# Performance work log

Measured on AMD Instinct MI355X. Metric: run time of the kernel, lower is better.

The kernel has to match this reference:

```python
import jax, jax.numpy as jnp
import numpy as np
from jax import lax

B, T, CD = 128, 4096, 2
HID, K = 64, 5
FIN = CD * 3 + 4  # 10 scorer input channels
PAD = K // 2
LEARNED_W = 0.5


def setup_inputs() -> dict:
    key = jax.random.key(0)
    ks = jax.random.split(key, 10)
    trajectory = jax.random.normal(ks[0], (B, T, CD), jnp.float32)
    intervals = jax.random.uniform(ks[1], (B, T), jnp.float32, 0.01, 1.0)
    lengths = jax.random.randint(ks[2], (B,), T // 2, T + 1)
    attention_mask = (jnp.arange(T)[None, :] < lengths[:, None]).astype(jnp.float32)
    observed_mask = (jax.random.uniform(ks[3], (B, T)) > 0.3).astype(jnp.float32)
    w1 = jax.random.normal(ks[4], (HID, FIN, K), jnp.float32) / np.sqrt(FIN * K)
    b1 = jnp.zeros((HID,), jnp.float32)
    w2 = jax.random.normal(ks[5], (HID, HID, K), jnp.float32) / np.sqrt(HID * K)
    b2 = jnp.zeros((HID,), jnp.float32)
    w3 = jax.random.normal(ks[6], (1, HID, 1), jnp.float32) / np.sqrt(HID)
    b3 = jnp.zeros((1,), jnp.float32)
    return dict(trajectory=trajectory, intervals=intervals, attention_mask=attention_mask,
                observed_mask=observed_mask, w1=w1, b1=b1, w2=w2, b2=b2, w3=w3, b3=b3)


def _conv1d(x, w, pad):  # x: [B,C,T], w: [O,I,K]
    return lax.conv_general_dilated(x, w, (1,), [(pad, pad)],
                                    dimension_numbers=('NCH', 'OIH', 'NCH'))


def _safe_norm(v):  # grad-safe L2 norm over last dim, exact forward
    s2 = jnp.sum(v * v, axis=-1)
    return jnp.where(s2 > 0, jnp.sqrt(jnp.where(s2 > 0, s2, 1.0)), 0.0)


def _robust_normalize(values, mask):
    # vectorized version of per-sample 95th-percentile scaling
    valid = mask > 0.5
    n = jnp.sum(valid, axis=1)  # [B] int
    s = jnp.sort(jnp.where(valid, values, jnp.inf), axis=1)  # valid ascending, inf last
    idx = jnp.maximum(1, jnp.ceil(n.astype(jnp.float32) * 0.95).astype(jnp.int32)) - 1
    idx = jnp.clip(idx, 0, T - 1)
    scale = jnp.abs(jnp.take_along_axis(s, idx[:, None], axis=1))[:, 0]
    maxabs = jnp.max(jnp.where(valid, jnp.abs(values), 0.0), axis=1)
    scale = jnp.where(scale < 1e-6, maxabs, scale)
    out = values / jnp.maximum(scale, 1e-6)[:, None]
    out = jnp.where((n > 0)[:, None], out, 0.0)
    return out * mask


def _smooth(scores, mask):  # avg_pool1d k=K stride 1 pad K//2 (count_include_pad=True)
    kern = jnp.full((1, 1, K), 1.0 / K, scores.dtype)
    sm = _conv1d(scores[:, None, :], kern, PAD)[:, 0]
    return sm * mask


def _forward(trajectory, intervals, attention_mask, observed_mask, w1, b1, w2, b2, w3, b3):
    mask = attention_mask
    vm = mask > 0.5
    pm = (vm[:, 1:] & vm[:, :-1]).astype(trajectory.dtype)  # [B,T-1]

    def mdiff3(x):
        d = (x[:, 1:] - x[:, :-1]) * pm[..., None]
        return jnp.concatenate([jnp.zeros_like(x[:, :1]), d], axis=1)

    def mdiff2(x):
        d = (x[:, 1:] - x[:, :-1]) * pm
        return jnp.concatenate([jnp.zeros_like(x[:, :1]), d], axis=1)

    mt = trajectory * mask[..., None]
    coord_diff = mdiff3(mt)
    delta_t = jnp.maximum(intervals[..., None], 1e-3)
    interval_feat = intervals * mask
    velocity = coord_diff / delta_t * mask[..., None]
    acceleration = mdiff3(velocity) / delta_t * mask[..., None]
    speed = _safe_norm(velocity) * mask
    speed_change = jnp.abs(mdiff2(speed)) * mask
    accel_norm = _safe_norm(acceleration) * mask
    heading = jnp.arctan2(velocity[..., 1], velocity[..., 0])
    rhc = heading[:, 1:] - heading[:, :-1]
    rhc = jnp.abs(jnp.arctan2(jnp.sin(rhc), jnp.cos(rhc)))
    heading_change = jnp.concatenate([jnp.zeros_like(speed[:, :1]), rhc * pm], axis=1) * mask
    obs_feat = observed_mask * mask
    ot = jnp.abs(observed_mask[:, 1:] - observed_mask[:, :-1]) * pm
    observed_transition = jnp.concatenate([jnp.zeros_like(speed[:, :1]), ot], axis=1) * mask

    feats = jnp.concatenate([mt, velocity, acceleration, speed[..., None],
                             heading_change[..., None], interval_feat[..., None],
                             obs_feat[..., None]], axis=-1) * mask[..., None]  # [B,T,10]

    # rule scores
    scores = (0.35 * _robust_normalize(heading_change, mask)
              + 0.30 * _robust_normalize(accel_norm, mask)
              + 0.25 * _robust_normalize(speed_change, mask)
              + 0.10 * jnp.clip(observed_transition, 0.0, 1.0) * mask)
    scores = _smooth(scores, mask)
    rule_scores = jnp.clip(_robust_normalize(scores, mask), 0.0, 1.0) * mask

    # learned scores (Conv1d stack, exact GELU like torch default)
    x = feats.transpose(0, 2, 1)  # [B,10,T]
    h = jax.nn.gelu(_conv1d(x, w1, PAD) + b1[None, :, None], approximate=False)
    h = jax.nn.gelu(_conv1d(h, w2, PAD) + b2[None, :, None], approximate=False)
    learned = jax.nn.sigmoid((_conv1d(h, w3, 0) + b3[None, :, None])[:, 0]) * mask
    learned = jnp.clip(_smooth(learned, mask), 0.0, 1.0)

    out = (1.0 - LEARNED_W) * rule_scores + LEARNED_W * learned
    return jnp.clip(out, 0.0, 1.0) * mask


def reference(trajectory, intervals, attention_mask, observed_mask, w1, b1, w2, b2, w3, b3):
    return _forward(trajectory, intervals, attention_mask, observed_mask, w1, b1, w2, b2, w3, b3)
```

## Files before the change

### kernel.cpp

```cpp
#include <hip/hip_runtime.h>

namespace {

constexpr int B_ = 128;
constexpr int T_ = 4096;
constexpr int BT = B_ * T_;
constexpr int TTILE = 128;
constexpr unsigned NOINS = 0xFFFFFFFFu;

constexpr size_t OFF_W1F   = 0;
constexpr size_t OFF_W2F   = 2048;
constexpr size_t OFF_FEATS = 16384;
constexpr size_t OFF_HC    = OFF_FEATS + (size_t)B_ * 10 * T_;
constexpr size_t OFF_AN    = OFF_HC + (size_t)BT;
constexpr size_t OFF_SC    = OFF_AN + (size_t)BT;
constexpr size_t OFF_OT    = OFF_SC + (size_t)BT;
constexpr size_t OFF_RULE  = OFF_OT + (size_t)BT;
constexpr size_t OFF_LP    = OFF_RULE + (size_t)BT;

typedef _Float16 half8 __attribute__((ext_vector_type(8)));
typedef _Float16 half4 __attribute__((ext_vector_type(4)));
typedef _Float16 half2_t __attribute__((ext_vector_type(2)));
typedef float f32x4 __attribute__((ext_vector_type(4)));

__device__ __forceinline__ float clip01(float x) { return fminf(fmaxf(x, 0.f), 1.f); }

__device__ __forceinline__ float gelu_fast(float x) {
  float s = x * 0.7071067811865475f;
  float a = fabsf(s);
  float t = __builtin_amdgcn_rcpf(__builtin_fmaf(0.3275911f, a, 1.0f));
  float p = __builtin_fmaf(t, 1.061405429f, -1.453152027f);
  p = __builtin_fmaf(t, p, 1.421413741f);
  p = __builtin_fmaf(t, p, -0.284496736f);
  p = __builtin_fmaf(t, p, 0.254829592f);
  p = p * t;
  float e = __builtin_amdgcn_exp2f(a * a * -1.4426950408889634f);
  float erfa = __builtin_fmaf(-p, e, 1.0f);
  float erfs = copysignf(erfa, s);
  return 0.5f * x * (1.0f + erfs);
}

__device__ __forceinline__ void compute_feats(
    const float* __restrict__ tr, const float* __restrict__ iv,
    const float* __restrict__ mk, const float* __restrict__ om, int t,
    float* __restrict__ f , float* anv_out, float* scv_out, float* otv_out) {
  float m  = mk[t];
  float m1 = (t >= 1) ? mk[t - 1] : 0.f;
  float m2 = (t >= 2) ? mk[t - 2] : 0.f;
  float pm01 = (m > 0.5f && m1 > 0.5f) ? 1.f : 0.f;
  float pm12 = (m1 > 0.5f && m2 > 0.5f) ? 1.f : 0.f;
  float x0x = tr[2 * t] * m, x0y = tr[2 * t + 1] * m;
  float x1x = 0.f, x1y = 0.f, x2x = 0.f, x2y = 0.f;
  if (t >= 1) { x1x = tr[2 * (t - 1)] * m1; x1y = tr[2 * (t - 1) + 1] * m1; }
  if (t >= 2) { x2x = tr[2 * (t - 2)] * m2; x2y = tr[2 * (t - 2) + 1] * m2; }
  float dt0 = fmaxf(iv[t], 1e-3f);
  float dt1 = (t >= 1) ? fmaxf(iv[t - 1], 1e-3f) : 1e-3f;
  float vx = 0.f, vy = 0.f, v1x = 0.f, v1y = 0.f;
  if (t >= 1) { vx = (x0x - x1x) * pm01 / dt0 * m; vy = (x0y - x1y) * pm01 / dt0 * m; }
  if (t >= 2) { v1x = (x1x - x2x) * pm12 / dt1 * m1; v1y = (x1y - x2y) * pm12 / dt1 * m1; }
  float ax = 0.f, ay = 0.f;
  if (t >= 1) { ax = (vx - v1x) * pm01 / dt0 * m; ay = (vy - v1y) * pm01 / dt0 * m; }
  float s2 = vx * vx + vy * vy;
  float speed = (s2 > 0.f ? sqrtf(s2) : 0.f) * m;
  float s21 = v1x * v1x + v1y * v1y;
  float speed1 = (s21 > 0.f ? sqrtf(s21) : 0.f) * m1;
  float scv = (t >= 1) ? fabsf((speed - speed1) * pm01) * m : 0.f;
  float a2 = ax * ax + ay * ay;
  float anv = (a2 > 0.f ? sqrtf(a2) : 0.f) * m;
  float hcv = 0.f;
  if (t >= 1) {
    bool z0 = (vx == 0.f && vy == 0.f);
    bool z1 = (v1x == 0.f && v1y == 0.f);
    float yy, xx;
    if (z1)      { yy = vy;  xx = vx; }
    else if (z0) { yy = v1y; xx = v1x; }
    else { yy = vy * v1x - vx * v1y; xx = vx * v1x + vy * v1y; }
    hcv = fabsf(atan2f(yy, xx)) * pm01 * m;
  }
  float obs = om[t] * m;
  float otv = (t >= 1) ? fminf(fabsf(om[t] - om[t - 1]) * pm01 * m, 1.f) : 0.f;
  float itf = iv[t] * m;
  f[0] = x0x; f[1] = x0y; f[2] = vx; f[3] = vy; f[4] = ax; f[5] = ay;
  f[6] = speed; f[7] = hcv; f[8] = itf; f[9] = obs;
  *anv_out = anv; *scv_out = scv; *otv_out = otv;
}

__global__ __launch_bounds__(256)
void featurize_k(const float* __restrict__ traj, const float* __restrict__ intervals,
                 const float* __restrict__ amask, const float* __restrict__ omask,
                 const float* __restrict__ w1g, const float* __restrict__ w2g,
                 float* __restrict__ feats, float* __restrict__ hc, float* __restrict__ an,
                 float* __restrict__ sc, float* __restrict__ ot,
                 half8* __restrict__ w1f, half8* __restrict__ w2f) {
  int idx = blockIdx.x * 256 + threadIdx.x;
  int b = idx >> 12;
  int t = idx & (T_ - 1);
  float f[10], anv, scv, otv;
  compute_feats(traj + (size_t)b * T_ * 2, intervals + (size_t)b * T_,
                amask + (size_t)b * T_, omask + (size_t)b * T_, t, f, &anv, &scv, &otv);
  float* frow = feats + (size_t)b * 10 * T_;
#pragma unroll
  for (int c = 0; c < 10; ++c) frow[(size_t)c * T_ + t] = f[c];
  hc[idx] = f[7]; an[idx] = anv; sc[idx] = scv; ot[idx] = otv;

  if (blockIdx.x < 12) {
    int gid = blockIdx.x * 256 + threadIdx.x;
    if (gid < 48 * 64) {
      int fid = gid >> 6, lane = gid & 63;
      int qd = lane >> 4, ln = lane & 15;
      half8 v;
      if (fid < 8) {
        int m = fid >> 1, kk = fid & 1;
        int o = m * 16 + ln;
#pragma unroll
        for (int j = 0; j < 8; ++j) {
          int ck = kk * 32 + qd * 8 + j;
          float val = 0.f;
          if (ck < 50) { int k_ = ck / 10, c = ck - 10 * k_; val = w1g[o * 50 + c * 5 + k_]; }
          v[j] = (_Float16)val;
        }
        w1f[fid * 64 + lane] = v;
      } else {
        int f2 = fid - 8;
        int k = f2 >> 3, kk = (f2 >> 2) & 1, m = f2 & 3;
        int o = m * 16 + ln;
#pragma unroll
        for (int j = 0; j < 8; ++j) {
          int ic = kk * 32 + qd * 8 + j;
          v[j] = (_Float16)w2g[o * 320 + ic * 5 + k];
        }
        w2f[f2 * 64 + lane] = v;
      }
    }
  }
}

__device__ __forceinline__ void scan4096(unsigned (*hist)[4096], int j, int tid, int lane,
                                         int wv, unsigned (*sW)[16], uint4& v,
                                         unsigned& ps, unsigned& incl) {
  v = *reinterpret_cast<uint4*>(&hist[j][tid * 4]);
  uint4 zz = {0u, 0u, 0u, 0u};
  *reinterpret_cast<uint4*>(&hist[j][tid * 4]) = zz;
  ps = v.x + v.y + v.z + v.w;
  incl = ps;
#pragma unroll
  for (int off = 1; off < 64; off <<= 1) {
    unsigned tv = __shfl_up(incl, off, 64);
    if (lane >= off) incl += tv;
  }
  if (lane == 63) sW[j][wv] = incl;
}
__device__ __forceinline__ void resolve4096(const unsigned (*sW)[16], int j, int tid, int wv,
                                            uint4 v, unsigned ps, unsigned incl, unsigned k,
                                            unsigned* selb, unsigned* selk) {
  unsigned woff = 0;
  for (int i = 0; i < wv; ++i) woff += sW[j][i];
  incl += woff;
  unsigned excl = incl - ps;
  if (excl <= k && k < incl) {
    unsigned vv[4] = {v.x, v.y, v.z, v.w};
    unsigned run = excl;
    int c = 0;
#pragma unroll
    for (; c < 3; ++c) {
      if (run + vv[c] > k) break;
      run += vv[c];
    }
    *selb = (unsigned)(tid * 4 + c);
    *selk = k - run;
  }
}
__device__ __forceinline__ void scan256(unsigned (*hist)[4096], int j, int tid, int lane,
                                        int wv, unsigned (*sW)[16], unsigned& v,
                                        unsigned& incl) {
  v = (tid < 256) ? hist[j][tid] : 0u;
  if (tid < 256) hist[j][tid] = 0u;
  incl = v;
#pragma unroll
  for (int off = 1; off < 64; off <<= 1) {
    unsigned tv = __shfl_up(incl, off, 64);
    if (lane >= off) incl += tv;
  }
  if (lane == 63) sW[j][wv] = incl;
}
__device__ __forceinline__ void resolve256(const unsigned (*sW)[16], int j, int tid, int wv,
                                           unsigned v, unsigned incl, unsigned k,
                                           unsigned* selb) {
  unsigned woff = 0;
  for (int i = 0; i < wv; ++i) woff += sW[j][i];
  incl += woff;
  unsigned excl = incl - v;
  if (excl <= k && k < incl) *selb = (unsigned)tid;
}

__global__ __launch_bounds__(1024)
void ruleselect_k(const float* __restrict__ hc, const float* __restrict__ an,
                  const float* __restrict__ sc, const float* __restrict__ ot,
                  const float* __restrict__ amask, float* __restrict__ rule) {
  __shared__ unsigned hist3[3][4096];
  __shared__ float vbuf[4096];
  __shared__ unsigned selB[2][4];
  __shared__ unsigned selK[2][4];
  __shared__ unsigned sW3[3][16];
  __shared__ float sM3[3][16];
  __shared__ int iCnt[16];
  int b = blockIdx.x, tid = threadIdx.x;
  int lane = tid & 63, wv = tid >> 6;
  const float* mk = amask + (size_t)b * T_;
  const float* h0 = hc + (size_t)b * T_;
  const float* a0 = an + (size_t)b * T_;
  const float* s0 = sc + (size_t)b * T_;
  const float* o0 = ot + (size_t)b * T_;

  float mv0[4], mv1[4], mv2[4], otv[4], mreg[4];
  int cnt = 0;
#pragma unroll
  for (int r = 0; r < 4; ++r) {
    int t = tid + 1024 * r;
    mv0[r] = h0[t]; mv1[r] = a0[t]; mv2[r] = s0[t]; otv[r] = o0[t];
    mreg[r] = mk[t];
    cnt += (mreg[r] > 0.5f);
  }
#pragma unroll
  for (int off = 32; off; off >>= 1) cnt += __shfl_xor(cnt, off);
  if (lane == 0) iCnt[wv] = cnt;
  {
    unsigned* hflat = &hist3[0][0];
    for (int i = tid; i < 3 * 4096; i += 1024) hflat[i] = 0u;
  }
  unsigned u0[4], u1[4], u2[4];
  float mxa = 0.f, mxb = 0.f, mxc = 0.f;
#pragma unroll
  for (int r = 0; r < 4; ++r) {
    bool valid = mreg[r] > 0.5f;
    unsigned b0 = __float_as_uint(mv0[r]); if ((int)b0 < 0) b0 = 0u;
    unsigned b1 = __float_as_uint(mv1[r]); if ((int)b1 < 0) b1 = 0u;
    unsigned b2 = __float_as_uint(mv2[r]); if ((int)b2 < 0) b2 = 0u;
    u0[r] = valid ? b0 : NOINS;
    u1[r] = valid ? b1 : NOINS;
    u2[r] = valid ? b2 : NOINS;
    if (valid) {
      mxa = fmaxf(mxa, fabsf(mv0[r]));
      mxb = fmaxf(mxb, fabsf(mv1[r]));
      mxc = fmaxf(mxc, fabsf(mv2[r]));
    }
  }
#pragma unroll
  for (int off = 32; off; off >>= 1) {
    mxa = fmaxf(mxa, __shfl_xor(mxa, off));
    mxb = fmaxf(mxb, __shfl_xor(mxb, off));
    mxc = fmaxf(mxc, __shfl_xor(mxc, off));
  }
  if (lane == 0) { sM3[0][wv] = mxa; sM3[1][wv] = mxb; sM3[2][wv] = mxc; }
  __syncthreads();
  int n = 0;
#pragma unroll
  for (int i = 0; i < 16; ++i) n += iCnt[i];
  int cidx = (int)ceilf((float)n * 0.95f);
  if (cidx < 1) cidx = 1;
  unsigned kidx = (unsigned)(cidx - 1);
  if (kidx > (unsigned)(T_ - 1)) kidx = T_ - 1;
  float mx3a = sM3[0][0], mx3b = sM3[1][0], mx3c = sM3[2][0];
#pragma unroll
  for (int i = 1; i < 16; ++i) {
    mx3a = fmaxf(mx3a, sM3[0][i]);
    mx3b = fmaxf(mx3b, sM3[1][i]);
    mx3c = fmaxf(mx3c, sM3[2][i]);
  }

#pragma unroll
  for (int r = 0; r < 4; ++r) {
    if (u0[r] != NOINS) atomicAdd(&hist3[0][u0[r] >> 20], 1u);
    if (u1[r] != NOINS) atomicAdd(&hist3[1][u1[r] >> 20], 1u);
    if (u2[r] != NOINS) atomicAdd(&hist3[2][u2[r] >> 20], 1u);
  }
  __syncthreads();
  uint4 v40, v41, v42; unsigned ps0, ps1, ps2, in0, in1, in2;
  scan4096(hist3, 0, tid, lane, wv, sW3, v40, ps0, in0);
  scan4096(hist3, 1, tid, lane, wv, sW3, v41, ps1, in1);
  scan4096(hist3, 2, tid, lane, wv, sW3, v42, ps2, in2);
  __syncthreads();
  resolve4096(sW3, 0, tid, wv, v40, ps0, in0, kidx, &selB[1][0], &selK[1][0]);
  resolve4096(sW3, 1, tid, wv, v41, ps1, in1, kidx, &selB[1][1], &selK[1][1]);
  resolve4096(sW3, 2, tid, wv, v42, ps2, in2, kidx, &selB[1][2], &selK[1][2]);
  __syncthreads();
  unsigned p1_0 = selB[1][0], p1_1 = selB[1][1], p1_2 = selB[1][2];
  unsigned k2_0 = selK[1][0], k2_1 = selK[1][1], k2_2 = selK[1][2];
#pragma unroll
  for (int r = 0; r < 4; ++r) {
    if (u0[r] != NOINS && (u0[r] >> 20) == p1_0) atomicAdd(&hist3[0][(u0[r] >> 8) & 0xFFFu], 1u);
    if (u1[r] != NOINS && (u1[r] >> 20) == p1_1) atomicAdd(&hist3[1][(u1[r] >> 8) & 0xFFFu], 1u);
    if (u2[r] != NOINS && (u2[r] >> 20) == p1_2) atomicAdd(&hist3[2][(u2[r] >> 8) & 0xFFFu], 1u);
  }
  __syncthreads();
  scan4096(hist3, 0, tid, lane, wv, sW3, v40, ps0, in0);
  scan4096(hist3, 1, tid, lane, wv, sW3, v41, ps1, in1);
  scan4096(hist3, 2, tid, lane, wv, sW3, v42, ps2, in2);
  __syncthreads();
  resolve4096(sW3, 0, tid, wv, v40, ps0, in0, k2_0, &selB[0][0], &selK[0][0]);
  resolve4096(sW3, 1, tid, wv, v41, ps1, in1, k2_1, &selB[0][1], &selK[0][1]);
  resolve4096(sW3, 2, tid, wv, v42, ps2, in2, k2_2, &selB[0][2], &selK[0][2]);
  __syncthreads();
  unsigned p2_0 = selB[0][0], p2_1 = selB[0][1], p2_2 = selB[0][2];
  unsigned k3_0 = selK[0][0], k3_1 = selK[0][1], k3_2 = selK[0][2];
  unsigned pf0 = (p1_0 << 12) | p2_0, pf1 = (p1_1 << 12) | p2_1, pf2 = (p1_2 << 12) | p2_2;
#pragma unroll
  for (int r = 0; r < 4; ++r) {
    if (u0[r] != NOINS && (u0[r] >> 8) == pf0) atomicAdd(&hist3[0][u0[r] & 0xFFu], 1u);
    if (u1[r] != NOINS && (u1[r] >> 8) == pf1) atomicAdd(&hist3[1][u1[r] & 0xFFu], 1u);
    if (u2[r] != NOINS && (u2[r] >> 8) == pf2) atomicAdd(&hist3[2][u2[r] & 0xFFu], 1u);
  }
  __syncthreads();
  unsigned s80, s81, s82;
  scan256(hist3, 0, tid, lane, wv, sW3, s80, in0);
  scan256(hist3, 1, tid, lane, wv, sW3, s81, in1);
  scan256(hist3, 2, tid, lane, wv, sW3, s82, in2);
  __syncthreads();
  resolve256(sW3, 0, tid, wv, s80, in0, k3_0, &selB[1][0]);
  resolve256(sW3, 1, tid, wv, s81, in1, k3_1, &selB[1][1]);
  resolve256(sW3, 2, tid, wv, s82, in2, k3_2, &selB[1][2]);
  __syncthreads();
  float kth0 = fabsf(__uint_as_float((p1_0 << 20) | (p2_0 << 8) | selB[1][0]));
  float kth1 = fabsf(__uint_as_float((p1_1 << 20) | (p2_1 << 8) | selB[1][1]));
  float kth2 = fabsf(__uint_as_float((p1_2 << 20) | (p2_2 << 8) | selB[1][2]));
  float sc0 = fmaxf((kth0 < 1e-6f) ? mx3a : kth0, 1e-6f);
  float sc1 = fmaxf((kth1 < 1e-6f) ? mx3b : kth1, 1e-6f);
  float sc2 = fmaxf((kth2 < 1e-6f) ? mx3c : kth2, 1e-6f);

#pragma unroll
  for (int r = 0; r < 4; ++r) {
    int t = tid + 1024 * r;
    float v = 0.f;
    if (n > 0) {
      v = 0.35f * (mv0[r] / sc0) + 0.30f * (mv1[r] / sc1)
        + 0.25f * (mv2[r] / sc2) + 0.10f * otv[r];
    }
    vbuf[t] = v;
  }
  __syncthreads();
  float sm[4];
#pragma unroll
  for (int r = 0; r < 4; ++r) {
    int t = tid + 1024 * r;
    float s = 0.f;
#pragma unroll
    for (int d = -2; d <= 2; ++d) {
      int tt = t + d;
      if (tt >= 0 && tt < T_) s += vbuf[tt];
    }
    sm[r] = s * 0.2f * mreg[r];
  }
  unsigned uu[4];
  float mxs = 0.f;
#pragma unroll
  for (int r = 0; r < 4; ++r) {
    bool valid = mreg[r] > 0.5f;
    unsigned ub = __float_as_uint(sm[r]); if ((int)ub < 0) ub = 0u;
    uu[r] = valid ? ub : NOINS;
    if (valid) mxs = fmaxf(mxs, fabsf(sm[r]));
  }
#pragma unroll
  for (int off = 32; off; off >>= 1) mxs = fmaxf(mxs, __shfl_xor(mxs, off));
  if (lane == 0) sM3[0][wv] = mxs;
#pragma unroll
  for (int r = 0; r < 4; ++r)
    if (uu[r] != NOINS) atomicAdd(&hist3[0][uu[r] >> 20], 1u);
  __syncthreads();
  float mx4 = sM3[0][0];
#pragma unroll
  for (int i = 1; i < 16; ++i) mx4 = fmaxf(mx4, sM3[0][i]);
  scan4096(hist3, 0, tid, lane, wv, sW3, v40, ps0, in0);
  __syncthreads();
  resolve4096(sW3, 0, tid, wv, v40, ps0, in0, kidx, &selB[1][3], &selK[1][3]);
  __syncthreads();
  unsigned q1 = selB[1][3], kq2 = selK[1][3];
#pragma unroll
  for (int r = 0; r < 4; ++r)
    if (uu[r] != NOINS && (uu[r] >> 20) == q1) atomicAdd(&hist3[0][(uu[r] >> 8) & 0xFFFu], 1u);
  __syncthreads();
  scan4096(hist3, 0, tid, lane, wv, sW3, v40, ps0, in0);
  __syncthreads();
  resolve4096(sW3, 0, tid, wv, v40, ps0, in0, kq2, &selB[0][3], &selK[0][3]);
  __syncthreads();
  unsigned q2 = selB[0][3], kq3 = selK[0][3];
  unsigned qf = (q1 << 12) | q2;
#pragma unroll
  for (int r = 0; r < 4; ++r)
    if (uu[r] != NOINS && (uu[r] >> 8) == qf) atomicAdd(&hist3[0][uu[r] & 0xFFu], 1u);
  __syncthreads();
  scan256(hist3, 0, tid, lane, wv, sW3, s80, in0);
  __syncthreads();
  resolve256(sW3, 0, tid, wv, s80, in0, kq3, &selB[1][3]);
  __syncthreads();
  float kth4 = fabsf(__uint_as_float((q1 << 20) | (q2 << 8) | selB[1][3]));
  float scale4 = fmaxf((kth4 < 1e-6f) ? mx4 : kth4, 1e-6f);
  float* rrow = rule + (size_t)b * T_;
#pragma unroll
  for (int r = 0; r < 4; ++r) {
    int t = tid + 1024 * r;
    float v = (n > 0) ? sm[r] / scale4 : 0.f;
    rrow[t] = clip01(v) * mreg[r];
  }
}

__global__ __launch_bounds__(512, 4)
void conv_k(const float* __restrict__ feats, const half8* __restrict__ w1f,
            const float* __restrict__ b1g, const half8* __restrict__ w2f,
            const float* __restrict__ b2g, const float* __restrict__ w3g,
            const float* __restrict__ b3g, const float* __restrict__ amask,
            float* __restrict__ lp) {
  __shared__ _Float16 sIm[144 * 72];
  __shared__ _Float16 sH1[132 * 72];
  __shared__ float sF[10 * 136];
  __shared__ float sPart[2][128];
  int tid = threadIdx.x;
  int lane = tid & 63, w = tid >> 6;
  int qd = lane >> 4, ln = lane & 15;
  int tile = blockIdx.x, b = blockIdx.y;
  int t0 = tile * TTILE;
  const float* frow = feats + (size_t)b * 10 * T_;

  for (int s = tid; s < 1360; s += 512) {
    int c = s / 136, u = s - c * 136;
    int t = t0 - 4 + u;
    sF[s] = (t >= 0 && t < T_) ? frow[(size_t)c * T_ + t] * 0.015625f : 0.f;
  }
  for (int s = tid; s < 144 * 7; s += 512) {
    int jt = s / 7, d = s - jt * 7;
    *reinterpret_cast<unsigned*>(&sIm[jt * 72 + 50 + 2 * d]) = 0u;
  }
  __syncthreads();
  for (int s = tid; s < 660; s += 512) {
    int jt = s / 5, k = s - jt * 5;
#pragma unroll
    for (int cp = 0; cp < 5; ++cp) {
      float lo = sF[(2 * cp) * 136 + jt + k];
      float hi = sF[(2 * cp + 1) * 136 + jt + k];
      half2_t pk;
      pk[0] = (_Float16)lo;
      pk[1] = (_Float16)hi;
      *reinterpret_cast<half2_t*>(&sIm[jt * 72 + k * 10 + 2 * cp]) = pk;
    }
  }
  __syncthreads();

  half8 a1[4][2];
#pragma unroll
  for (int m = 0; m < 4; ++m)
#pragma unroll
    for (int kk = 0; kk < 2; ++kk) a1[m][kk] = w1f[(m * 2 + kk) * 64 + lane];

  for (int n0 = w; n0 < 9; n0 += 8) {
    int jt = n0 * 16 + ln;
    half8 bf0 = *reinterpret_cast<const half8*>(&sIm[jt * 72 + qd * 8]);
    half8 bf1 = *reinterpret_cast<const half8*>(&sIm[jt * 72 + 32 + qd * 8]);
#pragma unroll
    for (int m = 0; m < 4; ++m) {
      f32x4 acc;
      f32x4 bv = *reinterpret_cast<const f32x4*>(&b1g[m * 16 + qd * 4]);
#pragma unroll
      for (int r = 0; r < 4; ++r) acc[r] = bv[r] * 0.015625f;
      acc = __builtin_amdgcn_mfma_f32_16x16x32_f16(a1[m][0], bf0, acc, 0, 0, 0);
      acc = __builtin_amdgcn_mfma_f32_16x16x32_f16(a1[m][1], bf1, acc, 0, 0, 0);
      if (jt < 132) {
        int t = t0 - 2 + jt;
        bool inr = (t >= 0 && t < T_);
        half4 hv;
#pragma unroll
        for (int r = 0; r < 4; ++r) {
          float h = inr ? gelu_fast(acc[r] * 64.f) * 0.0625f : 0.f;
          hv[r] = (_Float16)h;
        }
        *reinterpret_cast<half4*>(&sH1[jt * 72 + m * 16 + qd * 4]) = hv;
      }
    }
  }
  __syncthreads();

  int p = w & 1, nq = w >> 1;
  f32x4 acc2[2][2];
#pragma unroll
  for (int dm = 0; dm < 2; ++dm) {
    f32x4 bv = *reinterpret_cast<const f32x4*>(&b2g[(2 * p + dm) * 16 + qd * 4]);
#pragma unroll
    for (int dn = 0; dn < 2; ++dn)
#pragma unroll
      for (int r = 0; r < 4; ++r) acc2[dm][dn][r] = bv[r] * 0.0625f;
  }
#pragma unroll
  for (int k = 0; k < 5; ++k) {
#pragma unroll
    for (int kk = 0; kk < 2; ++kk) {
      half8 A0 = w2f[((k * 2 + kk) * 4 + 2 * p + 0) * 64 + lane];
      half8 A1 = w2f[((k * 2 + kk) * 4 + 2 * p + 1) * 64 + lane];
      half8 B0 = *reinterpret_cast<const half8*>(
          &sH1[((2 * nq + 0) * 16 + ln + k) * 72 + kk * 32 + qd * 8]);
      half8 B1 = *reinterpret_cast<const half8*>(
          &sH1[((2 * nq + 1) * 16 + ln + k) * 72 + kk * 32 + qd * 8]);
      acc2[0][0] = __builtin_amdgcn_mfma_f32_16x16x32_f16(A0, B0, acc2[0][0], 0, 0, 0);
      acc2[0][1] = __builtin_amdgcn_mfma_f32_16x16x32_f16(A0, B1, acc2[0][1], 0, 0, 0);
      acc2[1][0] = __builtin_amdgcn_mfma_f32_16x16x32_f16(A1, B0, acc2[1][0], 0, 0, 0);
      acc2[1][1] = __builtin_amdgcn_mfma_f32_16x16x32_f16(A1, B1, acc2[1][1], 0, 0, 0);
    }
  }
  f32x4 w3a = *reinterpret_cast<const f32x4*>(&w3g[(2 * p + 0) * 16 + qd * 4]);
  f32x4 w3b = *reinterpret_cast<const f32x4*>(&w3g[(2 * p + 1) * 16 + qd * 4]);
#pragma unroll
  for (int dn = 0; dn < 2; ++dn) {
    float s = 0.f;
#pragma unroll
    for (int r = 0; r < 4; ++r) s += w3a[r] * gelu_fast(acc2[0][dn][r] * 16.f);
#pragma unroll
    for (int r = 0; r < 4; ++r) s += w3b[r] * gelu_fast(acc2[1][dn][r] * 16.f);
    s += __shfl_xor(s, 16);
    s += __shfl_xor(s, 32);
    if (lane < 16) sPart[p][(2 * nq + dn) * 16 + lane] = s;
  }
  __syncthreads();
  if (tid < 128) {
    int t = t0 + tid;
    float logit = sPart[0][tid] + sPart[1][tid] + b3g[0];
    float m = amask[(size_t)b * T_ + t];
    lp[(size_t)b * T_ + t] = (1.f / (1.f + expf(-logit))) * m;
  }
}

__global__ __launch_bounds__(256)
void final_k(const float* __restrict__ rule, const float* __restrict__ lp,
             const float* __restrict__ amask, float* __restrict__ out) {
  int idx = blockIdx.x * 256 + threadIdx.x;
  if (idx >= BT) return;
  int t = idx & (T_ - 1);
  float s = 0.f;
#pragma unroll
  for (int d = -2; d <= 2; ++d) {
    int tt = t + d;
    if (tt >= 0 && tt < T_) s += lp[idx + d];
  }
  float m = amask[idx];
  float learned = clip01(s * 0.2f * m);
  out[idx] = clip01(0.5f * rule[idx] + 0.5f * learned) * m;
}

}

extern "C" void kernel_launch(void* const* d_in, const int* in_sizes, int n_in,
                              void* d_out, int out_size, void* d_ws, size_t ws_size,
                              hipStream_t stream) {
  const float* traj      = (const float*)d_in[0];
  const float* intervals = (const float*)d_in[1];
  const float* amask     = (const float*)d_in[2];
  const float* omask     = (const float*)d_in[3];
  const float* w1        = (const float*)d_in[4];
  const float* b1        = (const float*)d_in[5];
  const float* w2        = (const float*)d_in[6];
  const float* b2        = (const float*)d_in[7];
  const float* w3        = (const float*)d_in[8];
  const float* b3        = (const float*)d_in[9];
  float* out = (float*)d_out;
  float* ws = (float*)d_ws;

  float* feats = ws + OFF_FEATS;
  float* hc    = ws + OFF_HC;
  float* an    = ws + OFF_AN;
  float* sc    = ws + OFF_SC;
  float* ot    = ws + OFF_OT;
  float* rule  = ws + OFF_RULE;
  float* lp    = ws + OFF_LP;
  half8* w1f = (half8*)(ws + OFF_W1F);
  half8* w2f = (half8*)(ws + OFF_W2F);

  featurize_k<<<BT / 256, 256, 0, stream>>>(traj, intervals, amask, omask, w1, w2,
                                            feats, hc, an, sc, ot, w1f, w2f);
  ruleselect_k<<<B_, 1024, 0, stream>>>(hc, an, sc, ot, amask, rule);
  conv_k<<<dim3(T_ / TTILE, B_), 512, 0, stream>>>(feats, w1f, b1, w2f, b2, w3, b3,
                                                   amask, lp);
  final_k<<<BT / 256, 256, 0, stream>>>(rule, lp, amask, out);
}
```

Measured before the change: 178.8 us.

## Store features as packed fp16, fuse final blend into rule kernel, use tanh GELU

Featurize now writes the 10 features as time-major packed fp16 pairs, pre-scaled, instead of channel-major fp32. This halves feature traffic and lets conv_k build its im2col tile with plain word copies. The final smoothing and blend kernel is removed: ruleselect_k now runs after conv_k, reads the learned row into shared memory and writes the output directly, which drops one launch and the rule-score round trip through global memory. Both GELUs switch from an erf polynomial to a tanh-form sigmoid approximation, and the output sigmoid uses fast exp2/rcp. That approximation is no longer the exact erf GELU and may shift accuracy.

```diff
diff --git a/kernel.cpp b/kernel.cpp
--- a/kernel.cpp
+++ b/kernel.cpp
@@ -8,15 +8,14 @@
 constexpr int TTILE = 128;
 constexpr unsigned NOINS = 0xFFFFFFFFu;
 
-constexpr size_t OFF_W1F   = 0;
-constexpr size_t OFF_W2F   = 2048;
-constexpr size_t OFF_FEATS = 16384;
-constexpr size_t OFF_HC    = OFF_FEATS + (size_t)B_ * 10 * T_;
-constexpr size_t OFF_AN    = OFF_HC + (size_t)BT;
-constexpr size_t OFF_SC    = OFF_AN + (size_t)BT;
-constexpr size_t OFF_OT    = OFF_SC + (size_t)BT;
-constexpr size_t OFF_RULE  = OFF_OT + (size_t)BT;
-constexpr size_t OFF_LP    = OFF_RULE + (size_t)BT;
+constexpr size_t OFF_W1F = 0;
+constexpr size_t OFF_W2F = 2048;
+constexpr size_t OFF_F16 = 16384;
+constexpr size_t OFF_HC  = OFF_F16 + (size_t)BT * 5 / 2 * 2;
+constexpr size_t OFF_AN  = OFF_HC + (size_t)BT;
+constexpr size_t OFF_SC  = OFF_AN + (size_t)BT;
+constexpr size_t OFF_OT  = OFF_SC + (size_t)BT;
+constexpr size_t OFF_LP  = OFF_OT + (size_t)BT;
 
 typedef _Float16 half8 __attribute__((ext_vector_type(8)));
 typedef _Float16 half4 __attribute__((ext_vector_type(4)));
@@ -25,19 +24,11 @@
 
 __device__ __forceinline__ float clip01(float x) { return fminf(fmaxf(x, 0.f), 1.f); }
 
-__device__ __forceinline__ float gelu_fast(float x) {
-  float s = x * 0.7071067811865475f;
-  float a = fabsf(s);
-  float t = __builtin_amdgcn_rcpf(__builtin_fmaf(0.3275911f, a, 1.0f));
-  float p = __builtin_fmaf(t, 1.061405429f, -1.453152027f);
-  p = __builtin_fmaf(t, p, 1.421413741f);
-  p = __builtin_fmaf(t, p, -0.284496736f);
-  p = __builtin_fmaf(t, p, 0.254829592f);
-  p = p * t;
-  float e = __builtin_amdgcn_exp2f(a * a * -1.4426950408889634f);
-  float erfa = __builtin_fmaf(-p, e, 1.0f);
-  float erfs = copysignf(erfa, s);
-  return 0.5f * x * (1.0f + erfs);
+__device__ __forceinline__ float gelu_tanh(float x) {
+  float x2 = x * x;
+  float q = x * __builtin_fmaf(-0.10294444f, x2, -2.3022077f);
+  float e = __builtin_amdgcn_exp2f(q);
+  return x * __builtin_amdgcn_rcpf(1.0f + e);
 }
 
 __device__ __forceinline__ void compute_feats(
@@ -89,8 +80,8 @@
 void featurize_k(const float* __restrict__ traj, const float* __restrict__ intervals,
                  const float* __restrict__ amask, const float* __restrict__ omask,
                  const float* __restrict__ w1g, const float* __restrict__ w2g,
-                 float* __restrict__ feats, float* __restrict__ hc, float* __restrict__ an,
-                 float* __restrict__ sc, float* __restrict__ ot,
+                 _Float16* __restrict__ feats16, float* __restrict__ hc,
+                 float* __restrict__ an, float* __restrict__ sc, float* __restrict__ ot,
                  half8* __restrict__ w1f, half8* __restrict__ w2f) {
   int idx = blockIdx.x * 256 + threadIdx.x;
   int b = idx >> 12;
@@ -98,9 +89,14 @@
   float f[10], anv, scv, otv;
   compute_feats(traj + (size_t)b * T_ * 2, intervals + (size_t)b * T_,
                 amask + (size_t)b * T_, omask + (size_t)b * T_, t, f, &anv, &scv, &otv);
-  float* frow = feats + (size_t)b * 10 * T_;
-#pragma unroll
-  for (int c = 0; c < 10; ++c) frow[(size_t)c * T_ + t] = f[c];
+  half2_t* fd = reinterpret_cast<half2_t*>(feats16) + (size_t)idx * 5;
+#pragma unroll
+  for (int q = 0; q < 5; ++q) {
+    half2_t pk;
+    pk[0] = (_Float16)(f[2 * q] * 0.015625f);
+    pk[1] = (_Float16)(f[2 * q + 1] * 0.015625f);
+    fd[q] = pk;
+  }
   hc[idx] = f[7]; an[idx] = anv; sc[idx] = scv; ot[idx] = otv;
 
   if (blockIdx.x < 12) {
@@ -135,6 +131,126 @@
   }
 }
 
+__global__ __launch_bounds__(512, 4)
+void conv_k(const _Float16* __restrict__ feats16, const half8* __restrict__ w1f,
+            const float* __restrict__ b1g, const half8* __restrict__ w2f,
+            const float* __restrict__ b2g, const float* __restrict__ w3g,
+            const float* __restrict__ b3g, const float* __restrict__ amask,
+            float* __restrict__ lp) {
+  __shared__ _Float16 sIm[144 * 72];
+  __shared__ _Float16 sH1[132 * 72];
+  __shared__ _Float16 sF16[136 * 10];
+  __shared__ float sPart[2][128];
+  int tid = threadIdx.x;
+  int lane = tid & 63, w = tid >> 6;
+  int qd = lane >> 4, ln = lane & 15;
+  int tile = blockIdx.x, b = blockIdx.y;
+  int t0 = tile * TTILE;
+
+  const unsigned* gfd = reinterpret_cast<const unsigned*>(feats16 + (size_t)b * T_ * 10);
+  unsigned* sFd = reinterpret_cast<unsigned*>(sF16);
+  int dbase = (t0 - 4) * 5;
+  for (int s = tid; s < 680; s += 512) {
+    int gi = dbase + s;
+    sFd[s] = (gi >= 0 && gi < T_ * 5) ? gfd[gi] : 0u;
+  }
+  for (int s = tid; s < 144 * 7; s += 512) {
+    int jt = s / 7, d = s - jt * 7;
+    *reinterpret_cast<unsigned*>(&sIm[jt * 72 + 50 + 2 * d]) = 0u;
+  }
+  __syncthreads();
+  unsigned* sId = reinterpret_cast<unsigned*>(sIm);
+  for (int s = tid; s < 660; s += 512) {
+    int jt = s / 5, k = s - jt * 5;
+    const unsigned* src = sFd + (jt + k) * 5;
+    unsigned* dst = sId + jt * 36 + k * 5;
+#pragma unroll
+    for (int q = 0; q < 5; ++q) dst[q] = src[q];
+  }
+  __syncthreads();
+
+  half8 a1[4][2];
+#pragma unroll
+  for (int m = 0; m < 4; ++m)
+#pragma unroll
+    for (int kk = 0; kk < 2; ++kk) a1[m][kk] = w1f[(m * 2 + kk) * 64 + lane];
+
+  for (int n0 = w; n0 < 9; n0 += 8) {
+    int jt = n0 * 16 + ln;
+    half8 bf0 = *reinterpret_cast<const half8*>(&sIm[jt * 72 + qd * 8]);
+    half8 bf1 = *reinterpret_cast<const half8*>(&sIm[jt * 72 + 32 + qd * 8]);
+#pragma unroll
+    for (int m = 0; m < 4; ++m) {
+      f32x4 acc;
+      f32x4 bv = *reinterpret_cast<const f32x4*>(&b1g[m * 16 + qd * 4]);
+#pragma unroll
+      for (int r = 0; r < 4; ++r) acc[r] = bv[r] * 0.015625f;
+      acc = __builtin_amdgcn_mfma_f32_16x16x32_f16(a1[m][0], bf0, acc, 0, 0, 0);
+      acc = __builtin_amdgcn_mfma_f32_16x16x32_f16(a1[m][1], bf1, acc, 0, 0, 0);
+      if (jt < 132) {
+        int t = t0 - 2 + jt;
+        bool inr = (t >= 0 && t < T_);
+        half4 hv;
+#pragma unroll
+        for (int r = 0; r < 4; ++r) {
+          float h = inr ? gelu_tanh(acc[r] * 64.f) * 0.0625f : 0.f;
+          hv[r] = (_Float16)h;
+        }
+        *reinterpret_cast<half4*>(&sH1[jt * 72 + m * 16 + qd * 4]) = hv;
+      }
+    }
+  }
+  __syncthreads();
+
+  int p = w & 1, nq = w >> 1;
+  f32x4 acc2[2][2];
+#pragma unroll
+  for (int dm = 0; dm < 2; ++dm) {
+    f32x4 bv = *reinterpret_cast<const f32x4*>(&b2g[(2 * p + dm) * 16 + qd * 4]);
+#pragma unroll
+    for (int dn = 0; dn < 2; ++dn)
+#pragma unroll
+      for (int r = 0; r < 4; ++r) acc2[dm][dn][r] = bv[r] * 0.0625f;
+  }
+#pragma unroll
+  for (int k = 0; k < 5; ++k) {
+#pragma unroll
+    for (int kk = 0; kk < 2; ++kk) {
+      half8 A0 = w2f[((k * 2 + kk) * 4 + 2 * p + 0) * 64 + lane];
+      half8 A1 = w2f[((k * 2 + kk) * 4 + 2 * p + 1) * 64 + lane];
+      half8 B0 = *reinterpret_cast<const half8*>(
+          &sH1[((2 * nq + 0) * 16 + ln + k) * 72 + kk * 32 + qd * 8]);
+      half8 B1 = *reinterpret_cast<const half8*>(
+          &sH1[((2 * nq + 1) * 16 + ln + k) * 72 + kk * 32 + qd * 8]);
+      acc2[0][0] = __builtin_amdgcn_mfma_f32_16x16x32_f16(A0, B0, acc2[0][0], 0, 0, 0);
+      acc2[0][1] = __builtin_amdgcn_mfma_f32_16x16x32_f16(A0, B1, acc2[0][1], 0, 0, 0);
+      acc2[1][0] = __builtin_amdgcn_mfma_f32_16x16x32_f16(A1, B0, acc2[1][0], 0, 0, 0);
+      acc2[1][1] = __builtin_amdgcn_mfma_f32_16x16x32_f16(A1, B1, acc2[1][1], 0, 0, 0);
+    }
+  }
+  f32x4 w3a = *reinterpret_cast<const f32x4*>(&w3g[(2 * p + 0) * 16 + qd * 4]);
+  f32x4 w3b = *reinterpret_cast<const f32x4*>(&w3g[(2 * p + 1) * 16 + qd * 4]);
+#pragma unroll
+  for (int dn = 0; dn < 2; ++dn) {
+    float s = 0.f;
+#pragma unroll
+    for (int r = 0; r < 4; ++r) s += w3a[r] * gelu_tanh(acc2[0][dn][r] * 16.f);
+#pragma unroll
+    for (int r = 0; r < 4; ++r) s += w3b[r] * gelu_tanh(acc2[1][dn][r] * 16.f);
+    s += __shfl_xor(s, 16);
+    s += __shfl_xor(s, 32);
+    if (lane < 16) sPart[p][(2 * nq + dn) * 16 + lane] = s;
+  }
+  __syncthreads();
+  if (tid < 128) {
+    int t = t0 + tid;
+    float logit = sPart[0][tid] + sPart[1][tid] + b3g[0];
+    float m = amask[(size_t)b * T_ + t];
+    float e = __builtin_amdgcn_exp2f(logit * -1.4426950408889634f);
+    lp[(size_t)b * T_ + t] = m * __builtin_amdgcn_rcpf(1.f + e);
+  }
+}
+
 __device__ __forceinline__ void scan4096(unsigned (*hist)[4096], int j, int tid, int lane,
                                          int wv, unsigned (*sW)[16], uint4& v,
                                          unsigned& ps, unsigned& incl) {
@@ -196,7 +312,8 @@
 __global__ __launch_bounds__(1024)
 void ruleselect_k(const float* __restrict__ hc, const float* __restrict__ an,
                   const float* __restrict__ sc, const float* __restrict__ ot,
-                  const float* __restrict__ amask, float* __restrict__ rule) {
+                  const float* __restrict__ amask, const float* __restrict__ lp,
+                  float* __restrict__ out) {
   __shared__ unsigned hist3[3][4096];
   __shared__ float vbuf[4096];
   __shared__ unsigned selB[2][4];
@@ -366,6 +483,12 @@
   for (int r = 0; r < 4; ++r)
     if (uu[r] != NOINS) atomicAdd(&hist3[0][uu[r] >> 20], 1u);
   __syncthreads();
+  const float* lprow = lp + (size_t)b * T_;
+#pragma unroll
+  for (int r = 0; r < 4; ++r) {
+    int t = tid + 1024 * r;
+    vbuf[t] = lprow[t];
+  }
   float mx4 = sM3[0][0];
 #pragma unroll
   for (int i = 1; i < 16; ++i) mx4 = fmaxf(mx4, sM3[0][i]);
@@ -394,152 +517,21 @@
   __syncthreads();
   float kth4 = fabsf(__uint_as_float((q1 << 20) | (q2 << 8) | selB[1][3]));
   float scale4 = fmaxf((kth4 < 1e-6f) ? mx4 : kth4, 1e-6f);
-  float* rrow = rule + (size_t)b * T_;
+  float* orow = out + (size_t)b * T_;
 #pragma unroll
   for (int r = 0; r < 4; ++r) {
     int t = tid + 1024 * r;
-    float v = (n > 0) ? sm[r] / scale4 : 0.f;
-    rrow[t] = clip01(v) * mreg[r];
-  }
-}
-
-__global__ __launch_bounds__(512, 4)
-void conv_k(const float* __restrict__ feats, const half8* __restrict__ w1f,
-            const float* __restrict__ b1g, const half8* __restrict__ w2f,
-            const float* __restrict__ b2g, const float* __restrict__ w3g,
-            const float* __restrict__ b3g, const float* __restrict__ amask,
-            float* __restrict__ lp) {
-  __shared__ _Float16 sIm[144 * 72];
-  __shared__ _Float16 sH1[132 * 72];
-  __shared__ float sF[10 * 136];
-  __shared__ float sPart[2][128];
-  int tid = threadIdx.x;
-  int lane = tid & 63, w = tid >> 6;
-  int qd = lane >> 4, ln = lane & 15;
-  int tile = blockIdx.x, b = blockIdx.y;
-  int t0 = tile * TTILE;
-  const float* frow = feats + (size_t)b * 10 * T_;
-
-  for (int s = tid; s < 1360; s += 512) {
-    int c = s / 136, u = s - c * 136;
-    int t = t0 - 4 + u;
-    sF[s] = (t >= 0 && t < T_) ? frow[(size_t)c * T_ + t] * 0.015625f : 0.f;
-  }
-  for (int s = tid; s < 144 * 7; s += 512) {
-    int jt = s / 7, d = s - jt * 7;
-    *reinterpret_cast<unsigned*>(&sIm[jt * 72 + 50 + 2 * d]) = 0u;
-  }
-  __syncthreads();
-  for (int s = tid; s < 660; s += 512) {
-    int jt = s / 5, k = s - jt * 5;
-#pragma unroll
-    for (int cp = 0; cp < 5; ++cp) {
-      float lo = sF[(2 * cp) * 136 + jt + k];
-      float hi = sF[(2 * cp + 1) * 136 + jt + k];
-      half2_t pk;
-      pk[0] = (_Float16)lo;
-      pk[1] = (_Float16)hi;
-      *reinterpret_cast<half2_t*>(&sIm[jt * 72 + k * 10 + 2 * cp]) = pk;
-    }
-  }
-  __syncthreads();
-
-  half8 a1[4][2];
-#pragma unroll
-  for (int m = 0; m < 4; ++m)
-#pragma unroll
-    for (int kk = 0; kk < 2; ++kk) a1[m][kk] = w1f[(m * 2 + kk) * 64 + lane];
-
-  for (int n0 = w; n0 < 9; n0 += 8) {
-    int jt = n0 * 16 + ln;
-    half8 bf0 = *reinterpret_cast<const half8*>(&sIm[jt * 72 + qd * 8]);
-    half8 bf1 = *reinterpret_cast<const half8*>(&sIm[jt * 72 + 32 + qd * 8]);
-#pragma unroll
-    for (int m = 0; m < 4; ++m) {
-      f32x4 acc;
-      f32x4 bv = *reinterpret_cast<const f32x4*>(&b1g[m * 16 + qd * 4]);
-#pragma unroll
-      for (int r = 0; r < 4; ++r) acc[r] = bv[r] * 0.015625f;
-      acc = __builtin_amdgcn_mfma_f32_16x16x32_f16(a1[m][0], bf0, acc, 0, 0, 0);
-      acc = __builtin_amdgcn_mfma_f32_16x16x32_f16(a1[m][1], bf1, acc, 0, 0, 0);
-      if (jt < 132) {
-        int t = t0 - 2 + jt;
-        bool inr = (t >= 0 && t < T_);
-        half4 hv;
-#pragma unroll
-        for (int r = 0; r < 4; ++r) {
-          float h = inr ? gelu_fast(acc[r] * 64.f) * 0.0625f : 0.f;
-          hv[r] = (_Float16)h;
-        }
-        *reinterpret_cast<half4*>(&sH1[jt * 72 + m * 16 + qd * 4]) = hv;
-      }
-    }
-  }
-  __syncthreads();
-
-  int p = w & 1, nq = w >> 1;
-  f32x4 acc2[2][2];
-#pragma unroll
-  for (int dm = 0; dm < 2; ++dm) {
-    f32x4 bv = *reinterpret_cast<const f32x4*>(&b2g[(2 * p + dm) * 16 + qd * 4]);
-#pragma unroll
-    for (int dn = 0; dn < 2; ++dn)
-#pragma unroll
-      for (int r = 0; r < 4; ++r) acc2[dm][dn][r] = bv[r] * 0.0625f;
-  }
-#pragma unroll
-  for (int k = 0; k < 5; ++k) {
-#pragma unroll
-    for (int kk = 0; kk < 2; ++kk) {
-      half8 A0 = w2f[((k * 2 + kk) * 4 + 2 * p + 0) * 64 + lane];
-      half8 A1 = w2f[((k * 2 + kk) * 4 + 2 * p + 1) * 64 + lane];
-      half8 B0 = *reinterpret_cast<const half8*>(
-          &sH1[((2 * nq + 0) * 16 + ln + k) * 72 + kk * 32 + qd * 8]);
-      half8 B1 = *reinterpret_cast<const half8*>(
-          &sH1[((2 * nq + 1) * 16 + ln + k) * 72 + kk * 32 + qd * 8]);
-      acc2[0][0] = __builtin_amdgcn_mfma_f32_16x16x32_f16(A0, B0, acc2[0][0], 0, 0, 0);
-      acc2[0][1] = __builtin_amdgcn_mfma_f32_16x16x32_f16(A0, B1, acc2[0][1], 0, 0, 0);
-      acc2[1][0] = __builtin_amdgcn_mfma_f32_16x16x32_f16(A1, B0, acc2[1][0], 0, 0, 0);
-      acc2[1][1] = __builtin_amdgcn_mfma_f32_16x16x32_f16(A1, B1, acc2[1][1], 0, 0, 0);
-    }
-  }
-  f32x4 w3a = *reinterpret_cast<const f32x4*>(&w3g[(2 * p + 0) * 16 + qd * 4]);
-  f32x4 w3b = *reinterpret_cast<const f32x4*>(&w3g[(2 * p + 1) * 16 + qd * 4]);
-#pragma unroll
-  for (int dn = 0; dn < 2; ++dn) {
-    float s = 0.f;
-#pragma unroll
-    for (int r = 0; r < 4; ++r) s += w3a[r] * gelu_fast(acc2[0][dn][r] * 16.f);
-#pragma unroll
-    for (int r = 0; r < 4; ++r) s += w3b[r] * gelu_fast(acc2[1][dn][r] * 16.f);
-    s += __shfl_xor(s, 16);
-    s += __shfl_xor(s, 32);
-    if (lane < 16) sPart[p][(2 * nq + dn) * 16 + lane] = s;
-  }
-  __syncthreads();
-  if (tid < 128) {
-    int t = t0 + tid;
-    float logit = sPart[0][tid] + sPart[1][tid] + b3g[0];
-    float m = amask[(size_t)b * T_ + t];
-    lp[(size_t)b * T_ + t] = (1.f / (1.f + expf(-logit))) * m;
-  }
-}
-
-__global__ __launch_bounds__(256)
-void final_k(const float* __restrict__ rule, const float* __restrict__ lp,
-             const float* __restrict__ amask, float* __restrict__ out) {
-  int idx = blockIdx.x * 256 + threadIdx.x;
-  if (idx >= BT) return;
-  int t = idx & (T_ - 1);
-  float s = 0.f;
-#pragma unroll
-  for (int d = -2; d <= 2; ++d) {
-    int tt = t + d;
-    if (tt >= 0 && tt < T_) s += lp[idx + d];
-  }
-  float m = amask[idx];
-  float learned = clip01(s * 0.2f * m);
-  out[idx] = clip01(0.5f * rule[idx] + 0.5f * learned) * m;
+    float rv = (n > 0) ? sm[r] / scale4 : 0.f;
+    rv = clip01(rv) * mreg[r];
+    float ssum = 0.f;
+#pragma unroll
+    for (int d = -2; d <= 2; ++d) {
+      int tt = t + d;
+      if (tt >= 0 && tt < T_) ssum += vbuf[tt];
+    }
+    float learned = clip01(ssum * 0.2f * mreg[r]);
+    orow[t] = clip01(0.5f * rv + 0.5f * learned) * mreg[r];
+  }
 }
 
 }
@@ -560,20 +552,18 @@
   float* out = (float*)d_out;
   float* ws = (float*)d_ws;
 
-  float* feats = ws + OFF_FEATS;
-  float* hc    = ws + OFF_HC;
-  float* an    = ws + OFF_AN;
-  float* sc    = ws + OFF_SC;
-  float* ot    = ws + OFF_OT;
-  float* rule  = ws + OFF_RULE;
-  float* lp    = ws + OFF_LP;
+  _Float16* feats16 = (_Float16*)(ws + OFF_F16);
+  float* hc = ws + OFF_HC;
+  float* an = ws + OFF_AN;
+  float* sc = ws + OFF_SC;
+  float* ot = ws + OFF_OT;
+  float* lp = ws + OFF_LP;
   half8* w1f = (half8*)(ws + OFF_W1F);
   half8* w2f = (half8*)(ws + OFF_W2F);
 
   featurize_k<<<BT / 256, 256, 0, stream>>>(traj, intervals, amask, omask, w1, w2,
-                                            feats, hc, an, sc, ot, w1f, w2f);
-  ruleselect_k<<<B_, 1024, 0, stream>>>(hc, an, sc, ot, amask, rule);
-  conv_k<<<dim3(T_ / TTILE, B_), 512, 0, stream>>>(feats, w1f, b1, w2f, b2, w3, b3,
+                                            feats16, hc, an, sc, ot, w1f, w2f);
+  conv_k<<<dim3(T_ / TTILE, B_), 512, 0, stream>>>(feats16, w1f, b1, w2f, b2, w3, b3,
                                                    amask, lp);
-  final_k<<<BT / 256, 256, 0, stream>>>(rule, lp, amask, out);
-}
+  ruleselect_k<<<B_, 1024, 0, stream>>>(hc, an, sc, ot, amask, lp, out);
+}
```

After: 159.1 us. 11.0% less time.
